# Performance work log

Hardware: AMD Instinct MI355X
Metric: run time of the kernel (lower is better)

Reference implementation:

```python
import jax, jax.numpy as jnp
import numpy as np

B, C, L, H, T, W = 512, 256, 256, 512, 16, 8  # batch, num_channels, seq_len, hidden_dim, timestep, windows


def setup_inputs() -> dict:
    key = jax.random.key(0)
    ks = jax.random.split(key, 8)
    s = 0.02
    return {
        "features_aug2": jax.random.normal(ks[0], (B, C, L), jnp.float32),
        "c_t": jax.random.normal(ks[1], (B, W, H), jnp.float32),
        "Wk_w": jax.random.normal(ks[2], (T, C, H), jnp.float32) * s,
        "Wk_b": jnp.zeros((T, C), jnp.float32),
        "pw1": jax.random.normal(ks[3], (C // 2, H), jnp.float32) * s,
        "pb1": jnp.zeros((C // 2,), jnp.float32),
        "bn_gamma": jnp.ones((C // 2,), jnp.float32),
        "bn_beta": jnp.zeros((C // 2,), jnp.float32),
        "pw2": jax.random.normal(ks[4], (C // 4, C // 2), jnp.float32) * s,
        "pb2": jnp.zeros((C // 4,), jnp.float32),
        "t_sample": 100,
    }


def reference(features_aug2, c_t, Wk_w, Wk_b, pw1, pb1, bn_gamma, bn_beta, pw2, pb2, t_sample):
    z2 = jnp.transpose(features_aug2, (0, 2, 1))            # [B, L, C]
    seq_len = z2.shape[1]
    Tn, Cn = Wk_w.shape[0], Wk_w.shape[1]
    Wn = c_t.shape[1]
    Bn = c_t.shape[0]

    # encode_samples: window slices of z_aug2 at offsets t+1 .. t+T (clipped to seq end)
    starts = jnp.minimum(t_sample + 1 + jnp.arange(Tn), seq_len - Wn)  # [T]
    idx = starts[:, None] + jnp.arange(Wn)                   # [T, W]
    encode = jnp.transpose(z2[:, idx, :], (1, 0, 2, 3))      # [T, B, W, C]

    # pred[i] = Wk[i](c_t): batched linear over all timesteps
    pred = jnp.einsum('bwh,tch->tbwc', c_t, Wk_w) + Wk_b[:, None, None, :]  # [T, B, W, C]

    # fused InfoNCE: all T*W pairwise (B x B) score matrices at once
    scores = jnp.einsum('tbwc,tawc->twba', encode, pred)     # [T, W, B, B]
    logp = jax.nn.log_softmax(scores, axis=-1)               # LogSoftmax over dim=1 of each [B,B] (torch implicit dim)
    diag = jnp.diagonal(logp, axis1=-2, axis2=-1)            # [T, W, B]
    nce = -jnp.sum(diag) / (Bn * Tn * Wn)

    # projection head on c_t.reshape(-1, H): Linear -> BatchNorm1d (train stats) -> ReLU -> Linear
    x = c_t.reshape(-1, c_t.shape[-1])                       # [B*W, H]
    h1 = x @ pw1.T + pb1                                     # [B*W, C/2]
    mean = jnp.mean(h1, axis=0)
    var = jnp.mean((h1 - mean) ** 2, axis=0)                 # biased variance (BN train mode)
    h1 = (h1 - mean) * jax.lax.rsqrt(var + 1e-5) * bn_gamma + bn_beta
    h1 = jax.nn.relu(h1)
    proj = h1 @ pw2.T + pb2                                  # [B*W, C/4]
    return nce, proj
```

## Files before the change

### kernel.cpp

```cpp
#include <hip/hip_runtime.h>

#define B_SZ 512
#define C_CH 256
#define L_SEQ 256
#define H_DIM 512
#define T_STEP 16
#define W_WIN 8
#define NSLAB 24
#define NCE_SHIFT 40.0f

typedef __attribute__((ext_vector_type(8))) short short8;
typedef __attribute__((ext_vector_type(4))) float f32x4;

#define GLOBAL_U32 const __attribute__((address_space(1))) unsigned int*
#define LDS_U32 __attribute__((address_space(3))) unsigned int*
#define ASYNC_COPY16(g, l) \
  __builtin_amdgcn_global_load_lds((GLOBAL_U32)(const void*)(g), (LDS_U32)(void*)(l), 16, 0, 0)

__device__ inline unsigned short f2bf(float x) {
  unsigned u = __float_as_uint(x);
  u = (u + 0x7FFFu + ((u >> 16) & 1u)) >> 16;
  return (unsigned short)u;
}

__global__ void cast_bf(const float* __restrict__ s, unsigned short* __restrict__ d, int n) {
  int i = (blockIdx.x * 256 + threadIdx.x) * 4;
  if (i < n) {
    float4 v = ((const float4*)s)[i >> 2];
    ushort4 o;
    o.x = f2bf(v.x); o.y = f2bf(v.y); o.z = f2bf(v.z); o.w = f2bf(v.w);
    ((ushort4*)d)[i >> 2] = o;
  }
}

__global__ __launch_bounds__(256) void build_slabs2(const float* __restrict__ f,
                                                    unsigned short* __restrict__ F,
                                                    const int* __restrict__ tsp) {
  const int ts = tsp[0];
  const int lmin = min(ts + 1, L_SEQ - W_WIN);
  const int b = blockIdx.x;
  const int c = threadIdx.x;
  const float* src = f + ((size_t)b * C_CH + c) * L_SEQ;
  float v[NSLAB];
#pragma unroll
  for (int lp = 0; lp < NSLAB; lp++) {
    int l = lmin + lp;
    v[lp] = (l < L_SEQ) ? src[l] : 0.f;
  }
#pragma unroll
  for (int lp = 0; lp < NSLAB; lp++)
    F[((size_t)lp * B_SZ + b) * C_CH + c] = f2bf(v[lp]);
}

template <int MODE>
__global__ __launch_bounds__(256) void gemm_bt(const unsigned short* __restrict__ A,
                                               const unsigned short* __restrict__ Bt,
                                               const float* __restrict__ bias,
                                               unsigned short* __restrict__ outb,
                                               float* __restrict__ outf, int K) {
  __shared__ __align__(16) unsigned short As[128 * 64];
  __shared__ __align__(16) unsigned short Bs[128 * 64];
  const int tid = threadIdx.x;
  const int wv = tid >> 6, lane = tid & 63, quad = lane >> 4, l15 = lane & 15;
  const int wm = wv >> 1, wn = wv & 1;
  const int M0 = blockIdx.x * 128, N0 = blockIdx.y * 128;

  f32x4 acc[4][4];
#pragma unroll
  for (int i = 0; i < 4; i++)
#pragma unroll
    for (int j = 0; j < 4; j++) acc[i][j] = (f32x4){0.f, 0.f, 0.f, 0.f};

  for (int k0 = 0; k0 < K; k0 += 64) {
#pragma unroll
    for (int i = 0; i < 4; i++) {
      int chunk = (i * 4 + wv) * 64 + lane;
      int row = chunk >> 3, off = chunk & 7;
      const unsigned short* ga = A + (size_t)(M0 + row) * K + k0 + off * 8;
      const unsigned short* gb = Bt + (size_t)(N0 + row) * K + k0 + off * 8;
      ASYNC_COPY16(ga, &As[(size_t)(i * 4 + wv) * 512]);
      ASYNC_COPY16(gb, &Bs[(size_t)(i * 4 + wv) * 512]);
    }
    __syncthreads();
#pragma unroll
    for (int kk = 0; kk < 64; kk += 32) {
      short8 af[4], bfr[4];
#pragma unroll
      for (int i = 0; i < 4; i++)
        af[i] = *(const short8*)&As[(wm * 64 + i * 16 + l15) * 64 + kk + quad * 8];
#pragma unroll
      for (int j = 0; j < 4; j++)
        bfr[j] = *(const short8*)&Bs[(wn * 64 + j * 16 + l15) * 64 + kk + quad * 8];
#pragma unroll
      for (int i = 0; i < 4; i++)
#pragma unroll
        for (int j = 0; j < 4; j++)
          acc[i][j] = __builtin_amdgcn_mfma_f32_16x16x32_bf16(af[i], bfr[j], acc[i][j], 0, 0, 0);
    }
    __syncthreads();
  }

#pragma unroll
  for (int i = 0; i < 4; i++) {
    int rbase = M0 + wm * 64 + i * 16 + quad * 4;
#pragma unroll
    for (int j = 0; j < 4; j++) {
      int cc = N0 + wn * 64 + j * 16 + l15;
      float bv = bias[cc];
#pragma unroll
      for (int r = 0; r < 4; r++) {
        int rr = rbase + r;
        float v = acc[i][j][r] + bv;
        if (MODE == 0) {
          int t = cc >> 8, c = cc & 255, a = rr >> 3, w_ = rr & 7;
          outb[((size_t)(t * 8 + w_) * 512 + a) * 256 + c] = f2bf(v);
        } else {
          outf[(size_t)rr * 128 + cc] = v;
        }
      }
    }
  }
}

__global__ __launch_bounds__(256) void scores_gemm(const unsigned short* __restrict__ F,
                                                   const unsigned short* __restrict__ pred,
                                                   const int* __restrict__ tsp,
                                                   float* __restrict__ rowsum,
                                                   float* __restrict__ diagv) {
  __shared__ __align__(16) unsigned short As[128 * 64];
  __shared__ __align__(16) unsigned short Bs[128 * 64];
  const int tid = threadIdx.x;
  const int wv = tid >> 6, lane = tid & 63, quad = lane >> 4, l15 = lane & 15;
  const int wm = wv >> 1, wn = wv & 1;
  const int rowblk = blockIdx.x, colblk = blockIdx.y, tw = blockIdx.z;
  const int t = tw >> 3, w_ = tw & 7;
  const int ts = tsp[0];
  const int lmin = min(ts + 1, L_SEQ - W_WIN);
  const int lp = min(ts + 1 + t, L_SEQ - W_WIN) + w_ - lmin;
  const unsigned short* A = F + (size_t)lp * (B_SZ * C_CH) + (size_t)rowblk * 128 * C_CH;
  const unsigned short* Bt = pred + (size_t)tw * (B_SZ * C_CH) + (size_t)colblk * 128 * C_CH;

  f32x4 acc[4][4];
#pragma unroll
  for (int i = 0; i < 4; i++)
#pragma unroll
    for (int j = 0; j < 4; j++) acc[i][j] = (f32x4){0.f, 0.f, 0.f, 0.f};

  for (int k0 = 0; k0 < C_CH; k0 += 64) {
#pragma unroll
    for (int i = 0; i < 4; i++) {
      int chunk = (i * 4 + wv) * 64 + lane;
      int row = chunk >> 3, off = chunk & 7;
      ASYNC_COPY16(A + (size_t)row * C_CH + k0 + off * 8, &As[(size_t)(i * 4 + wv) * 512]);
      ASYNC_COPY16(Bt + (size_t)row * C_CH + k0 + off * 8, &Bs[(size_t)(i * 4 + wv) * 512]);
    }
    __syncthreads();
#pragma unroll
    for (int kk = 0; kk < 64; kk += 32) {
      short8 af[4], bfr[4];
#pragma unroll
      for (int i = 0; i < 4; i++)
        af[i] = *(const short8*)&As[(wm * 64 + i * 16 + l15) * 64 + kk + quad * 8];
#pragma unroll
      for (int j = 0; j < 4; j++)
        bfr[j] = *(const short8*)&Bs[(wn * 64 + j * 16 + l15) * 64 + kk + quad * 8];
#pragma unroll
      for (int i = 0; i < 4; i++)
#pragma unroll
        for (int j = 0; j < 4; j++)
          acc[i][j] = __builtin_amdgcn_mfma_f32_16x16x32_bf16(af[i], bfr[j], acc[i][j], 0, 0, 0);
    }
    __syncthreads();
  }

#pragma unroll
  for (int i = 0; i < 4; i++) {
#pragma unroll
    for (int r = 0; r < 4; r++) {
      float e = 0.f;
#pragma unroll
      for (int j = 0; j < 4; j++) e += __expf(acc[i][j][r] - NCE_SHIFT);
      e += __shfl_xor(e, 1);
      e += __shfl_xor(e, 2);
      e += __shfl_xor(e, 4);
      e += __shfl_xor(e, 8);
      if (l15 == 0) {
        int b = rowblk * 128 + wm * 64 + i * 16 + quad * 4 + r;
        atomicAdd(&rowsum[(size_t)tw * B_SZ + b], e);
      }
    }
  }
  if (rowblk == colblk && wm == wn) {
#pragma unroll
    for (int i = 0; i < 4; i++)
#pragma unroll
      for (int r = 0; r < 4; r++)
        if (l15 == quad * 4 + r) {
          int b = rowblk * 128 + wm * 64 + i * 16 + quad * 4 + r;
          diagv[(size_t)tw * B_SZ + b] = acc[i][i][r];
        }
  }
}

__global__ __launch_bounds__(256) void nce_rows(const float* __restrict__ rowsum,
                                                const float* __restrict__ diagv,
                                                float* __restrict__ parts) {
  int gid = blockIdx.x * 256 + threadIdx.x;
  float s = 0.f;
  for (int i = gid; i < 65536; i += 16384)
    s += logf(rowsum[i]) + NCE_SHIFT - diagv[i];
  __shared__ float r[256];
  r[threadIdx.x] = s;
  __syncthreads();
  if (threadIdx.x == 0) {
    float t = 0.f;
    for (int k = 0; k < 256; k++) t += r[k];
    parts[blockIdx.x] = t;
  }
}

__global__ void nce_out(const float* __restrict__ parts, float* __restrict__ out) {
  if (threadIdx.x == 0) {
    float t = 0.f;
    for (int k = 0; k < 64; k++) t += parts[k];
    out[0] = t / 65536.0f;
  }
}

__global__ void bn_stage1(const float* __restrict__ h1, float* __restrict__ p1,
                          float* __restrict__ p2) {
  int c = threadIdx.x;
  int blk = blockIdx.x;
  float s1 = 0.f, s2 = 0.f;
  for (int r = blk * 128; r < blk * 128 + 128; r++) {
    float v = h1[(size_t)r * 128 + c];
    s1 += v;
    s2 += v * v;
  }
  p1[blk * 128 + c] = s1;
  p2[blk * 128 + c] = s2;
}

__global__ void bn_stage2(const float* __restrict__ p1, const float* __restrict__ p2,
                          const float* __restrict__ g, const float* __restrict__ b,
                          float* __restrict__ sc, float* __restrict__ sh) {
  int c = threadIdx.x;
  float s1 = 0.f, s2 = 0.f;
  for (int k = 0; k < 32; k++) {
    s1 += p1[k * 128 + c];
    s2 += p2[k * 128 + c];
  }
  float mean = s1 * (1.f / 4096.f);
  float var = s2 * (1.f / 4096.f) - mean * mean;
  float scale = g[c] * rsqrtf(var + 1e-5f);
  sc[c] = scale;
  sh[c] = b[c] - mean * scale;
}

__global__ __launch_bounds__(256) void proj_gemm2(const float* __restrict__ h1,
                                                  const float* __restrict__ sc,
                                                  const float* __restrict__ sh,
                                                  const float* __restrict__ pw2,
                                                  const float* __restrict__ pb2,
                                                  float* __restrict__ out) {
  __shared__ float pw2s[64][129];
  __shared__ float hs[16][129];
  __shared__ float scs[128], shs[128];
  int tid = threadIdx.x;
  for (int idx = tid; idx < 64 * 128; idx += 256) pw2s[idx >> 7][idx & 127] = pw2[idx];
  if (tid < 128) { scs[tid] = sc[tid]; shs[tid] = sh[tid]; }
  __syncthreads();
  int r0 = blockIdx.x * 64;
  float bb = pb2[tid & 63];
  for (int ch = 0; ch < 4; ch++) {
    int rr0 = r0 + ch * 16;
    for (int idx = tid; idx < 16 * 128; idx += 256) {
      int r = idx >> 7, c = idx & 127;
      float v = h1[(size_t)(rr0 + r) * 128 + c];
      hs[r][c] = fmaxf(v * scs[c] + shs[c], 0.f);
    }
    __syncthreads();
    int oc = tid & 63, og = tid >> 6;
#pragma unroll
    for (int q = 0; q < 4; q++) {
      int row = og * 4 + q;
      float s = bb;
      for (int c = 0; c < 128; c++) s += hs[row][c] * pw2s[oc][c];
      out[(size_t)(rr0 + row) * 64 + oc] = s;
    }
    __syncthreads();
  }
}

extern "C" void kernel_launch(void* const* d_in, const int* in_sizes, int n_in,
                              void* d_out, int out_size, void* d_ws, size_t ws_size,
                              hipStream_t stream) {
  const float* features = (const float*)d_in[0];
  const float* c_t      = (const float*)d_in[1];
  const float* Wk_w     = (const float*)d_in[2];
  const float* Wk_b     = (const float*)d_in[3];
  const float* pw1      = (const float*)d_in[4];
  const float* pb1      = (const float*)d_in[5];
  const float* bn_gamma = (const float*)d_in[6];
  const float* bn_beta  = (const float*)d_in[7];
  const float* pw2      = (const float*)d_in[8];
  const float* pb2      = (const float*)d_in[9];
  const int*   tsp      = (const int*)d_in[10];
  float* out = (float*)d_out;

  char* ws = (char*)d_ws;
  size_t off = 0;
  auto carve = [&](size_t bytes) { void* p = ws + off; off += (bytes + 255) & ~(size_t)255; return p; };
  unsigned short* ct_bf  = (unsigned short*)carve((size_t)4096 * 512 * 2);
  unsigned short* wk_bf  = (unsigned short*)carve((size_t)4096 * 512 * 2);
  unsigned short* pw1_bf = (unsigned short*)carve((size_t)128 * 512 * 2);
  unsigned short* F      = (unsigned short*)carve((size_t)NSLAB * 512 * 256 * 2);
  unsigned short* pred   = (unsigned short*)carve((size_t)16 * 8 * 512 * 256 * 2);
  float* h1     = (float*)carve((size_t)4096 * 128 * 4);
  float* bnp1   = (float*)carve((size_t)32 * 128 * 4);
  float* bnp2   = (float*)carve((size_t)32 * 128 * 4);
  float* bnsc   = (float*)carve((size_t)128 * 4);
  float* bnsh   = (float*)carve((size_t)128 * 4);
  float* parts  = (float*)carve((size_t)2048 * 4);
  float* rowsum = (float*)carve((size_t)65536 * 4);
  float* diagv  = (float*)carve((size_t)65536 * 4);

  cast_bf<<<2048, 256, 0, stream>>>(c_t, ct_bf, 4096 * 512);
  cast_bf<<<2048, 256, 0, stream>>>(Wk_w, wk_bf, 4096 * 512);
  cast_bf<<<64, 256, 0, stream>>>(pw1, pw1_bf, 128 * 512);
  build_slabs2<<<512, 256, 0, stream>>>(features, F, tsp);
  hipMemsetAsync(rowsum, 0, (size_t)65536 * 4, stream);

  gemm_bt<0><<<dim3(32, 32), 256, 0, stream>>>(ct_bf, wk_bf, Wk_b, pred, nullptr, 512);
  gemm_bt<1><<<dim3(32, 1), 256, 0, stream>>>(ct_bf, pw1_bf, pb1, nullptr, h1, 512);

  scores_gemm<<<dim3(4, 4, 128), 256, 0, stream>>>(F, pred, tsp, rowsum, diagv);
  nce_rows<<<64, 256, 0, stream>>>(rowsum, diagv, parts);
  nce_out<<<1, 64, 0, stream>>>(parts, out);

  bn_stage1<<<32, 128, 0, stream>>>(h1, bnp1, bnp2);
  bn_stage2<<<1, 128, 0, stream>>>(bnp1, bnp2, bn_gamma, bn_beta, bnsc, bnsh);
  proj_gemm2<<<64, 256, 0, stream>>>(h1, bnsc, bnsh, pw2, pb2, out + 1);
}
```

Measured before the change: 332.1 us.

## Fuse prep casts, BN stats into GEMM epilogue, swizzle grids, drop atomics

Merges the three cast kernels and the zeroing into a single prep launch. The BN sum and sum-of-squares move into the h1 GEMM epilogue, and the two BN stage kernels plus nce_out are removed. GEMM and scores blocks are remapped through an XCD-style swizzle so neighbouring tiles land on the same die. Scores rowsum atomics become per-column-block partial writes that nce_rows sums, and the projection GEMM is rewritten with a register-tiled 4x4 outer product. These cut launch count, memset and atomic contention, at the cost of float atomics on the output and BN stats, which makes reduction order nondeterministic.

```diff
diff --git a/kernel.cpp b/kernel.cpp
--- a/kernel.cpp
+++ b/kernel.cpp
@@ -23,14 +23,32 @@
   return (unsigned short)u;
 }
 
-__global__ void cast_bf(const float* __restrict__ s, unsigned short* __restrict__ d, int n) {
-  int i = (blockIdx.x * 256 + threadIdx.x) * 4;
-  if (i < n) {
-    float4 v = ((const float4*)s)[i >> 2];
-    ushort4 o;
-    o.x = f2bf(v.x); o.y = f2bf(v.y); o.z = f2bf(v.z); o.w = f2bf(v.w);
-    ((ushort4*)d)[i >> 2] = o;
-  }
+__global__ __launch_bounds__(256) void prep(const float* __restrict__ ct,
+                                            const float* __restrict__ wk,
+                                            const float* __restrict__ pw1,
+                                            unsigned short* __restrict__ ctb,
+                                            unsigned short* __restrict__ wkb,
+                                            unsigned short* __restrict__ pw1b,
+                                            float* __restrict__ bnp1,
+                                            float* __restrict__ bnp2,
+                                            float* __restrict__ out) {
+  int b = blockIdx.x;
+  if (b == 4160) {
+    if (threadIdx.x < 128) { bnp1[threadIdx.x] = 0.f; bnp2[threadIdx.x] = 0.f; }
+    if (threadIdx.x == 0) out[0] = 0.f;
+    return;
+  }
+  const float* s;
+  unsigned short* d;
+  int base;
+  if (b < 2048)      { s = ct;  d = ctb;  base = b * 1024; }
+  else if (b < 4096) { s = wk;  d = wkb;  base = (b - 2048) * 1024; }
+  else               { s = pw1; d = pw1b; base = (b - 4096) * 1024; }
+  int i = base + threadIdx.x * 4;
+  float4 v = ((const float4*)s)[i >> 2];
+  ushort4 o;
+  o.x = f2bf(v.x); o.y = f2bf(v.y); o.z = f2bf(v.z); o.w = f2bf(v.w);
+  ((ushort4*)d)[i >> 2] = o;
 }
 
 __global__ __launch_bounds__(256) void build_slabs2(const float* __restrict__ f,
@@ -57,13 +75,23 @@
                                                const unsigned short* __restrict__ Bt,
                                                const float* __restrict__ bias,
                                                unsigned short* __restrict__ outb,
-                                               float* __restrict__ outf, int K) {
+                                               float* __restrict__ outf,
+                                               float* __restrict__ bnp1,
+                                               float* __restrict__ bnp2, int K) {
   __shared__ __align__(16) unsigned short As[128 * 64];
   __shared__ __align__(16) unsigned short Bs[128 * 64];
   const int tid = threadIdx.x;
   const int wv = tid >> 6, lane = tid & 63, quad = lane >> 4, l15 = lane & 15;
   const int wm = wv >> 1, wn = wv & 1;
-  const int M0 = blockIdx.x * 128, N0 = blockIdx.y * 128;
+  int M0, N0;
+  if (MODE == 0) {
+    int swz = (blockIdx.x & 7) * 128 + (blockIdx.x >> 3);
+    M0 = (swz >> 5) * 128;
+    N0 = (swz & 31) * 128;
+  } else {
+    M0 = blockIdx.x * 128;
+    N0 = 0;
+  }
 
   f32x4 acc[4][4];
 #pragma unroll
@@ -100,6 +128,9 @@
     __syncthreads();
   }
 
+  float st1[4], st2[4];
+#pragma unroll
+  for (int j = 0; j < 4; j++) { st1[j] = 0.f; st2[j] = 0.f; }
 #pragma unroll
   for (int i = 0; i < 4; i++) {
     int rbase = M0 + wm * 64 + i * 16 + quad * 4;
@@ -116,8 +147,28 @@
           outb[((size_t)(t * 8 + w_) * 512 + a) * 256 + c] = f2bf(v);
         } else {
           outf[(size_t)rr * 128 + cc] = v;
+          st1[j] += v;
+          st2[j] += v * v;
         }
       }
+    }
+  }
+  if (MODE == 1) {
+    __shared__ float red1[2][128], red2[2][128];
+#pragma unroll
+    for (int j = 0; j < 4; j++) {
+      float a1 = st1[j], a2 = st2[j];
+      a1 += __shfl_xor(a1, 16); a1 += __shfl_xor(a1, 32);
+      a2 += __shfl_xor(a2, 16); a2 += __shfl_xor(a2, 32);
+      if (quad == 0) {
+        red1[wm][wn * 64 + j * 16 + l15] = a1;
+        red2[wm][wn * 64 + j * 16 + l15] = a2;
+      }
+    }
+    __syncthreads();
+    if (tid < 128) {
+      atomicAdd(&bnp1[tid], red1[0][tid] + red1[1][tid]);
+      atomicAdd(&bnp2[tid], red2[0][tid] + red2[1][tid]);
     }
   }
 }
@@ -125,14 +176,15 @@
 __global__ __launch_bounds__(256) void scores_gemm(const unsigned short* __restrict__ F,
                                                    const unsigned short* __restrict__ pred,
                                                    const int* __restrict__ tsp,
-                                                   float* __restrict__ rowsum,
+                                                   float* __restrict__ rowsum_p,
                                                    float* __restrict__ diagv) {
   __shared__ __align__(16) unsigned short As[128 * 64];
   __shared__ __align__(16) unsigned short Bs[128 * 64];
   const int tid = threadIdx.x;
   const int wv = tid >> 6, lane = tid & 63, quad = lane >> 4, l15 = lane & 15;
   const int wm = wv >> 1, wn = wv & 1;
-  const int rowblk = blockIdx.x, colblk = blockIdx.y, tw = blockIdx.z;
+  const int swz = (blockIdx.x & 7) * 256 + (blockIdx.x >> 3);
+  const int tw = swz >> 4, rowblk = (swz >> 2) & 3, colblk = swz & 3;
   const int t = tw >> 3, w_ = tw & 7;
   const int ts = tsp[0];
   const int lmin = min(ts + 1, L_SEQ - W_WIN);
@@ -186,7 +238,7 @@
       e += __shfl_xor(e, 8);
       if (l15 == 0) {
         int b = rowblk * 128 + wm * 64 + i * 16 + quad * 4 + r;
-        atomicAdd(&rowsum[(size_t)tw * B_SZ + b], e);
+        rowsum_p[((size_t)tw * 8 + colblk * 2 + wn) * B_SZ + b] = e;
       }
     }
   }
@@ -202,93 +254,74 @@
   }
 }
 
-__global__ __launch_bounds__(256) void nce_rows(const float* __restrict__ rowsum,
+__global__ __launch_bounds__(256) void nce_rows(const float* __restrict__ rowsum_p,
                                                 const float* __restrict__ diagv,
-                                                float* __restrict__ parts) {
+                                                float* __restrict__ out) {
   int gid = blockIdx.x * 256 + threadIdx.x;
   float s = 0.f;
-  for (int i = gid; i < 65536; i += 16384)
-    s += logf(rowsum[i]) + NCE_SHIFT - diagv[i];
-  __shared__ float r[256];
-  r[threadIdx.x] = s;
+  for (int i = gid; i < 65536; i += 16384) {
+    int tw = i >> 9, b = i & 511;
+    float rs = 0.f;
+#pragma unroll
+    for (int p = 0; p < 8; p++) rs += rowsum_p[((size_t)tw * 8 + p) * B_SZ + b];
+    s += logf(rs) + NCE_SHIFT - diagv[i];
+  }
+#pragma unroll
+  for (int off = 1; off < 64; off <<= 1) s += __shfl_xor(s, off);
+  __shared__ float r[4];
+  if ((threadIdx.x & 63) == 0) r[threadIdx.x >> 6] = s;
   __syncthreads();
-  if (threadIdx.x == 0) {
-    float t = 0.f;
-    for (int k = 0; k < 256; k++) t += r[k];
-    parts[blockIdx.x] = t;
-  }
-}
-
-__global__ void nce_out(const float* __restrict__ parts, float* __restrict__ out) {
-  if (threadIdx.x == 0) {
-    float t = 0.f;
-    for (int k = 0; k < 64; k++) t += parts[k];
-    out[0] = t / 65536.0f;
-  }
-}
-
-__global__ void bn_stage1(const float* __restrict__ h1, float* __restrict__ p1,
-                          float* __restrict__ p2) {
-  int c = threadIdx.x;
-  int blk = blockIdx.x;
-  float s1 = 0.f, s2 = 0.f;
-  for (int r = blk * 128; r < blk * 128 + 128; r++) {
-    float v = h1[(size_t)r * 128 + c];
-    s1 += v;
-    s2 += v * v;
-  }
-  p1[blk * 128 + c] = s1;
-  p2[blk * 128 + c] = s2;
-}
-
-__global__ void bn_stage2(const float* __restrict__ p1, const float* __restrict__ p2,
-                          const float* __restrict__ g, const float* __restrict__ b,
-                          float* __restrict__ sc, float* __restrict__ sh) {
-  int c = threadIdx.x;
-  float s1 = 0.f, s2 = 0.f;
-  for (int k = 0; k < 32; k++) {
-    s1 += p1[k * 128 + c];
-    s2 += p2[k * 128 + c];
-  }
-  float mean = s1 * (1.f / 4096.f);
-  float var = s2 * (1.f / 4096.f) - mean * mean;
-  float scale = g[c] * rsqrtf(var + 1e-5f);
-  sc[c] = scale;
-  sh[c] = b[c] - mean * scale;
-}
-
-__global__ __launch_bounds__(256) void proj_gemm2(const float* __restrict__ h1,
-                                                  const float* __restrict__ sc,
-                                                  const float* __restrict__ sh,
-                                                  const float* __restrict__ pw2,
-                                                  const float* __restrict__ pb2,
-                                                  float* __restrict__ out) {
-  __shared__ float pw2s[64][129];
-  __shared__ float hs[16][129];
+  if (threadIdx.x == 0)
+    atomicAdd(out, (r[0] + r[1] + r[2] + r[3]) * (1.f / 65536.f));
+}
+
+__global__ __launch_bounds__(256) void proj2(const float* __restrict__ h1,
+                                             const float* __restrict__ bnp1,
+                                             const float* __restrict__ bnp2,
+                                             const float* __restrict__ g,
+                                             const float* __restrict__ bta,
+                                             const float* __restrict__ pw2,
+                                             const float* __restrict__ pb2,
+                                             float* __restrict__ out) {
+  __shared__ float hsT[128][68];
+  __shared__ float pw2T[128][68];
   __shared__ float scs[128], shs[128];
-  int tid = threadIdx.x;
-  for (int idx = tid; idx < 64 * 128; idx += 256) pw2s[idx >> 7][idx & 127] = pw2[idx];
-  if (tid < 128) { scs[tid] = sc[tid]; shs[tid] = sh[tid]; }
+  const int tid = threadIdx.x;
+  for (int idx = tid; idx < 64 * 128; idx += 256) {
+    int oc = idx >> 7, k = idx & 127;
+    pw2T[k][oc] = pw2[idx];
+  }
+  if (tid < 128) {
+    float mean = bnp1[tid] * (1.f / 4096.f);
+    float var = bnp2[tid] * (1.f / 4096.f) - mean * mean;
+    float scale = g[tid] * rsqrtf(var + 1e-5f);
+    scs[tid] = scale;
+    shs[tid] = bta[tid] - mean * scale;
+  }
   __syncthreads();
-  int r0 = blockIdx.x * 64;
-  float bb = pb2[tid & 63];
-  for (int ch = 0; ch < 4; ch++) {
-    int rr0 = r0 + ch * 16;
-    for (int idx = tid; idx < 16 * 128; idx += 256) {
-      int r = idx >> 7, c = idx & 127;
-      float v = h1[(size_t)(rr0 + r) * 128 + c];
-      hs[r][c] = fmaxf(v * scs[c] + shs[c], 0.f);
-    }
-    __syncthreads();
-    int oc = tid & 63, og = tid >> 6;
-#pragma unroll
-    for (int q = 0; q < 4; q++) {
-      int row = og * 4 + q;
-      float s = bb;
-      for (int c = 0; c < 128; c++) s += hs[row][c] * pw2s[oc][c];
-      out[(size_t)(rr0 + row) * 64 + oc] = s;
-    }
-    __syncthreads();
+  const int r0 = blockIdx.x * 64;
+  for (int idx = tid; idx < 64 * 128; idx += 256) {
+    int r = idx >> 7, k = idx & 127;
+    float v = h1[(size_t)(r0 + r) * 128 + k];
+    hsT[k][r] = fmaxf(v * scs[k] + shs[k], 0.f);
+  }
+  __syncthreads();
+  const int tx = tid & 15, ty = tid >> 4;
+  float acc[4][4] = {};
+  for (int k = 0; k < 128; k++) {
+    f32x4 hv = *(const f32x4*)&hsT[k][ty * 4];
+    f32x4 wv = *(const f32x4*)&pw2T[k][tx * 4];
+#pragma unroll
+    for (int i = 0; i < 4; i++)
+#pragma unroll
+      for (int j = 0; j < 4; j++) acc[i][j] += hv[i] * wv[j];
+  }
+#pragma unroll
+  for (int i = 0; i < 4; i++) {
+    int rr = r0 + ty * 4 + i;
+#pragma unroll
+    for (int j = 0; j < 4; j++)
+      out[(size_t)rr * 64 + tx * 4 + j] = acc[i][j] + pb2[tx * 4 + j];
   }
 }
 
@@ -316,29 +349,20 @@
   unsigned short* pw1_bf = (unsigned short*)carve((size_t)128 * 512 * 2);
   unsigned short* F      = (unsigned short*)carve((size_t)NSLAB * 512 * 256 * 2);
   unsigned short* pred   = (unsigned short*)carve((size_t)16 * 8 * 512 * 256 * 2);
-  float* h1     = (float*)carve((size_t)4096 * 128 * 4);
-  float* bnp1   = (float*)carve((size_t)32 * 128 * 4);
-  float* bnp2   = (float*)carve((size_t)32 * 128 * 4);
-  float* bnsc   = (float*)carve((size_t)128 * 4);
-  float* bnsh   = (float*)carve((size_t)128 * 4);
-  float* parts  = (float*)carve((size_t)2048 * 4);
-  float* rowsum = (float*)carve((size_t)65536 * 4);
-  float* diagv  = (float*)carve((size_t)65536 * 4);
-
-  cast_bf<<<2048, 256, 0, stream>>>(c_t, ct_bf, 4096 * 512);
-  cast_bf<<<2048, 256, 0, stream>>>(Wk_w, wk_bf, 4096 * 512);
-  cast_bf<<<64, 256, 0, stream>>>(pw1, pw1_bf, 128 * 512);
+  float* h1       = (float*)carve((size_t)4096 * 128 * 4);
+  float* bnp1     = (float*)carve((size_t)128 * 4);
+  float* bnp2     = (float*)carve((size_t)128 * 4);
+  float* rowsum_p = (float*)carve((size_t)128 * 8 * 512 * 4);
+  float* diagv    = (float*)carve((size_t)65536 * 4);
+
+  prep<<<4161, 256, 0, stream>>>(c_t, Wk_w, pw1, ct_bf, wk_bf, pw1_bf, bnp1, bnp2, out);
   build_slabs2<<<512, 256, 0, stream>>>(features, F, tsp);
-  hipMemsetAsync(rowsum, 0, (size_t)65536 * 4, stream);
-
-  gemm_bt<0><<<dim3(32, 32), 256, 0, stream>>>(ct_bf, wk_bf, Wk_b, pred, nullptr, 512);
-  gemm_bt<1><<<dim3(32, 1), 256, 0, stream>>>(ct_bf, pw1_bf, pb1, nullptr, h1, 512);
-
-  scores_gemm<<<dim3(4, 4, 128), 256, 0, stream>>>(F, pred, tsp, rowsum, diagv);
-  nce_rows<<<64, 256, 0, stream>>>(rowsum, diagv, parts);
-  nce_out<<<1, 64, 0, stream>>>(parts, out);
-
-  bn_stage1<<<32, 128, 0, stream>>>(h1, bnp1, bnp2);
-  bn_stage2<<<1, 128, 0, stream>>>(bnp1, bnp2, bn_gamma, bn_beta, bnsc, bnsh);
-  proj_gemm2<<<64, 256, 0, stream>>>(h1, bnsc, bnsh, pw2, pb2, out + 1);
-}
+
+  gemm_bt<0><<<1024, 256, 0, stream>>>(ct_bf, wk_bf, Wk_b, pred, nullptr, nullptr, nullptr, 512);
+  gemm_bt<1><<<32, 256, 0, stream>>>(ct_bf, pw1_bf, pb1, nullptr, h1, bnp1, bnp2, 512);
+
+  scores_gemm<<<2048, 256, 0, stream>>>(F, pred, tsp, rowsum_p, diagv);
+  nce_rows<<<64, 256, 0, stream>>>(rowsum_p, diagv, out);
+
+  proj2<<<64, 256, 0, stream>>>(h1, bnp1, bnp2, bn_gamma, bn_beta, pw2, pb2, out + 1);
+}
```

New measurement: 296.8 us. 10.6% less time.
